# Kernel optimization log

Measured on AMD Instinct MI355X. Metric: run time of the kernel, lower is better.

## Reference

```python
import jax, jax.numpy as jnp
import numpy as np

D = 256      # input channels
DK = 64      # key/query/value channels
BS, W, H = 8, 64, 64


def setup_inputs() -> dict:
    key = jax.random.key(0)
    k1, k2, k3, k4 = jax.random.split(key, 4)
    v = jax.random.normal(k1, (BS, D, W, H), dtype=jnp.float32)
    # conv1x1 weights collapse to plain matrices over the channel dim
    Wqkv = jax.random.normal(k2, (3 * DK, D), dtype=jnp.float32) * 0.02
    Wout = jax.random.normal(k3, (D, DK), dtype=jnp.float32) * 0.02
    gamma = jax.random.normal(k4, (1,), dtype=jnp.float32)  # original inits to 0; nonzero for a non-degenerate baseline
    return {"v": v, "Wqkv": Wqkv, "Wout": Wout, "gamma": gamma}


def reference(v, Wqkv, Wout, gamma):
    bs, c, w, h = v.shape
    n = w * h
    d_k = Wout.shape[1]
    x = v.reshape(bs, c, n)                      # (b, c, n)
    qkv = jnp.einsum('oc,bcn->bon', Wqkv, x)      # 1x1 conv == channel matmul
    q = qkv[:, :d_k]                              # (b, dk, n)
    k = qkv[:, d_k:2 * d_k]
    val = qkv[:, 2 * d_k:]
    s = jnp.einsum('bdi,bdj->bij', q, k)          # (b, n, n) = query^T key
    beta = jax.nn.softmax(s, axis=2)              # exp(s - logsumexp(s, axis=2))
    y = jnp.einsum('bdi,bij->bdj', val, beta)     # bmm(value, beta)
    o = jnp.einsum('od,bdn->bon', Wout, y) * gamma[0] + x
    return o.reshape(bs, c, w, h)
```

## Files before the change

### kernel.cpp

```cpp
#include <hip/hip_runtime.h>

typedef unsigned short ushort_t;
typedef __bf16 bf16x8 __attribute__((ext_vector_type(8)));
typedef short short4v __attribute__((ext_vector_type(4)));
typedef float f32x4 __attribute__((ext_vector_type(4)));
typedef unsigned int uint4v __attribute__((ext_vector_type(4)));
typedef unsigned int uint2v __attribute__((ext_vector_type(2)));

#define NTOK 4096
#define DMODEL 256
#define DK 64
#define BS 8
#define LN2INV 1.44269504088896f

__device__ __forceinline__ ushort_t f2bf(float f) {
  unsigned u = __builtin_bit_cast(unsigned, f);
  u += 0x7fffu + ((u >> 16) & 1u);
  return (ushort_t)(u >> 16);
}
__device__ __forceinline__ float bf2f(ushort_t s) {
  return __builtin_bit_cast(float, ((unsigned)s) << 16);
}
__device__ __forceinline__ bf16x8 lds_frag(const ushort_t* p) {
  return __builtin_bit_cast(bf16x8, *(const uint4v*)p);
}
__device__ __forceinline__ float fexp2(float x) {
#if __has_builtin(__builtin_amdgcn_exp2f)
  return __builtin_amdgcn_exp2f(x);
#else
  return exp2f(x);
#endif
}
__device__ __forceinline__ unsigned bfpack(float x, float y) {
  return __builtin_amdgcn_perm(__builtin_bit_cast(unsigned, y),
                               __builtin_bit_cast(unsigned, x), 0x07060302u);
}
__device__ __forceinline__ f32x4 mfma16(short4v a, short4v b, f32x4 c) {
#if defined(__HIP_DEVICE_COMPILE__)
#if __has_builtin(__builtin_amdgcn_mfma_f32_16x16x16bf16_1k)
  return __builtin_amdgcn_mfma_f32_16x16x16bf16_1k(a, b, c, 0, 0, 0);
#else
  typedef __bf16 bf16x4 __attribute__((ext_vector_type(4)));
  return __builtin_amdgcn_mfma_f32_16x16x16_bf16(__builtin_bit_cast(bf16x4, a),
                                                 __builtin_bit_cast(bf16x4, b), c, 0, 0, 0);
#endif
#else
  (void)a; (void)b;
  return c;
#endif
}

__global__ __launch_bounds__(256) void k_convert(const float* __restrict__ Wqkv,
                                                 const float* __restrict__ Wout,
                                                 ushort_t* __restrict__ Wb,
                                                 ushort_t* __restrict__ Woutb) {
  int i = blockIdx.x * 256 + threadIdx.x;
  if (i < 3 * DK * DMODEL) {
    float w = Wqkv[i];
    if (i < DK * DMODEL) w *= LN2INV;
    Wb[i] = f2bf(w);
  } else {
    int j = i - 3 * DK * DMODEL;
    Woutb[j] = f2bf(Wout[j]);
  }
}

__global__ __launch_bounds__(256) void k_transpose(const float* __restrict__ x,
                                                   ushort_t* __restrict__ xT) {
  const int b = blockIdx.z;
  const int c0 = blockIdx.y * 64;
  const int n0 = blockIdx.x * 64;
  const int tid = threadIdx.x;
  __shared__ __align__(16) ushort_t t[64 * 72];
  const float* xb = x + (size_t)b * DMODEL * NTOK;
  ushort_t* xTb = xT + (size_t)b * NTOK * DMODEL;
#pragma unroll
  for (int kr = 0; kr < 2; kr++) {
    int s = tid + 256 * kr;
    int c = s >> 3, ns = (s & 7) * 8;
    const float* src = xb + (size_t)(c0 + c) * NTOK + n0 + ns;
    f32x4 a = *(const f32x4*)src;
    f32x4 bq = *(const f32x4*)(src + 4);
    uint4v o;
    o.x = (unsigned)f2bf(a[0]) | ((unsigned)f2bf(a[1]) << 16);
    o.y = (unsigned)f2bf(a[2]) | ((unsigned)f2bf(a[3]) << 16);
    o.z = (unsigned)f2bf(bq[0]) | ((unsigned)f2bf(bq[1]) << 16);
    o.w = (unsigned)f2bf(bq[2]) | ((unsigned)f2bf(bq[3]) << 16);
    *(uint4v*)(t + c * 72 + ns) = o;
  }
  __syncthreads();
#pragma unroll
  for (int kr = 0; kr < 2; kr++) {
    int s = tid + 256 * kr;
    int n = s >> 3, cs = (s & 7) * 8;
    unsigned e0 = t[(cs + 0) * 72 + n], e1 = t[(cs + 1) * 72 + n];
    unsigned e2 = t[(cs + 2) * 72 + n], e3 = t[(cs + 3) * 72 + n];
    unsigned e4 = t[(cs + 4) * 72 + n], e5 = t[(cs + 5) * 72 + n];
    unsigned e6 = t[(cs + 6) * 72 + n], e7 = t[(cs + 7) * 72 + n];
    uint4v o;
    o.x = e0 | (e1 << 16); o.y = e2 | (e3 << 16);
    o.z = e4 | (e5 << 16); o.w = e6 | (e7 << 16);
    *(uint4v*)(xTb + (size_t)(n0 + n) * DMODEL + c0 + cs) = o;
  }
}

__global__ __launch_bounds__(256) void k_qkv(const ushort_t* __restrict__ xT,
                                             const ushort_t* __restrict__ W,
                                             ushort_t* __restrict__ QT,
                                             ushort_t* __restrict__ KT,
                                             ushort_t* __restrict__ Vv) {
  const int b = blockIdx.y;
  const int n0 = blockIdx.x * 64;
  const int tid = threadIdx.x;
  const int lane = tid & 63, wv = tid >> 6;
  const int quad = lane >> 4, l15 = lane & 15;
  __shared__ __align__(16) ushort_t lw[192 * 40];
  __shared__ __align__(16) ushort_t lx[64 * 40];
  f32x4 acc[3][4];
  const f32x4 zero4 = {0.f, 0.f, 0.f, 0.f};
#pragma unroll
  for (int i = 0; i < 3; i++)
#pragma unroll
    for (int j = 0; j < 4; j++) acc[i][j] = zero4;

  const ushort_t* xTb = xT + ((size_t)b * NTOK + n0) * DMODEL;

  for (int c0 = 0; c0 < DMODEL; c0 += 32) {
    __syncthreads();
#pragma unroll
    for (int kr = 0; kr < 3; kr++) {
      int s = tid + 256 * kr;
      int o = s >> 2, cs = (s & 3) * 8;
      *(uint4v*)(lw + o * 40 + cs) = *(const uint4v*)(W + o * DMODEL + c0 + cs);
    }
    {
      int n = tid >> 2, cs = (tid & 3) * 8;
      *(uint4v*)(lx + n * 40 + cs) = *(const uint4v*)(xTb + (size_t)n * DMODEL + c0 + cs);
    }
    __syncthreads();
    bf16x8 bb[4];
#pragma unroll
    for (int nt = 0; nt < 4; nt++) bb[nt] = lds_frag(lx + (nt * 16 + l15) * 40 + quad * 8);
#pragma unroll
    for (int mt = 0; mt < 3; mt++) {
      bf16x8 a = lds_frag(lw + (wv * 48 + mt * 16 + l15) * 40 + quad * 8);
#pragma unroll
      for (int nt = 0; nt < 4; nt++)
        acc[mt][nt] = __builtin_amdgcn_mfma_f32_16x16x32_bf16(a, bb[nt], acc[mt][nt], 0, 0, 0);
    }
  }
#pragma unroll
  for (int mt = 0; mt < 3; mt++) {
    int o = wv * 48 + mt * 16 + quad * 4;
#pragma unroll
    for (int nt = 0; nt < 4; nt++) {
      int n = n0 + nt * 16 + l15;
      f32x4 v4 = acc[mt][nt];
      if (o < 128) {
        ushort_t* dst = (o < 64) ? (QT + ((size_t)b * NTOK + n) * DK + o)
                                 : (KT + ((size_t)b * NTOK + n) * DK + (o - 64));
        uint2v ww;
        ww.x = (unsigned)f2bf(v4[0]) | ((unsigned)f2bf(v4[1]) << 16);
        ww.y = (unsigned)f2bf(v4[2]) | ((unsigned)f2bf(v4[3]) << 16);
        *(uint2v*)dst = ww;
      } else {
        int d = o - 128;
#pragma unroll
        for (int r = 0; r < 4; r++)
          Vv[((size_t)b * DK + d + r) * NTOK + n] = f2bf(v4[r]);
      }
    }
  }
}

__global__ __launch_bounds__(256) void k_rsum(const ushort_t* __restrict__ QT,
                                              const ushort_t* __restrict__ KT,
                                              float* __restrict__ Rp) {
  const int id = blockIdx.x;
  const int b = id & 7;
  const int rest = id >> 3;
  const int i0 = (rest & 63) * 64;
  const int jh = rest >> 6;
  const int tid = threadIdx.x;
  const int lane = tid & 63, wv = tid >> 6;
  const int quad = lane >> 4, l15 = lane & 15;
  __shared__ __align__(16) ushort_t lq[64 * 72];
  __shared__ __align__(16) ushort_t lk[2][64 * 72];
  const ushort_t* QTb = QT + ((size_t)b * NTOK + i0) * DK;
  const ushort_t* KTb = KT + ((size_t)b * NTOK + jh * 2048) * DK;
#pragma unroll
  for (int kr = 0; kr < 2; kr++) {
    int s = tid + 256 * kr;
    int row = s >> 3, ds = (s & 7) * 8;
    *(uint4v*)(lq + row * 72 + ds) = *(const uint4v*)(QTb + (size_t)row * DK + ds);
    *(uint4v*)(lk[0] + row * 72 + ds) = *(const uint4v*)(KTb + (size_t)row * DK + ds);
  }
  __syncthreads();
  bf16x8 a0 = lds_frag(lq + (wv * 16 + l15) * 72 + quad * 8);
  bf16x8 a1 = lds_frag(lq + (wv * 16 + l15) * 72 + 32 + quad * 8);
  float lsum0 = 0.f, lsum1 = 0.f, lsum2 = 0.f, lsum3 = 0.f;
  const f32x4 zero4 = {0.f, 0.f, 0.f, 0.f};
  for (int it = 0; it < 32; it++) {
    if (it + 1 < 32) {
      const ushort_t* src = KTb + (size_t)(it + 1) * 64 * DK;
      ushort_t* dstb = lk[(it + 1) & 1];
#pragma unroll
      for (int kr = 0; kr < 2; kr++) {
        int s = tid + 256 * kr;
        int row = s >> 3, ds = (s & 7) * 8;
        *(uint4v*)(dstb + row * 72 + ds) = *(const uint4v*)(src + (size_t)row * DK + ds);
      }
    }
    const ushort_t* kb = lk[it & 1];
#pragma unroll
    for (int nt = 0; nt < 4; nt++) {
      bf16x8 b0 = lds_frag(kb + (nt * 16 + l15) * 72 + quad * 8);
      bf16x8 b1 = lds_frag(kb + (nt * 16 + l15) * 72 + 32 + quad * 8);
      f32x4 s4 = __builtin_amdgcn_mfma_f32_16x16x32_bf16(a0, b0, zero4, 0, 0, 0);
      s4 = __builtin_amdgcn_mfma_f32_16x16x32_bf16(a1, b1, s4, 0, 0, 0);
      lsum0 += fexp2(s4[0]);
      lsum1 += fexp2(s4[1]);
      lsum2 += fexp2(s4[2]);
      lsum3 += fexp2(s4[3]);
    }
    __syncthreads();
  }
#pragma unroll
  for (int off = 1; off < 16; off <<= 1) {
    lsum0 += __shfl_xor(lsum0, off);
    lsum1 += __shfl_xor(lsum1, off);
    lsum2 += __shfl_xor(lsum2, off);
    lsum3 += __shfl_xor(lsum3, off);
  }
  if (l15 < 4) {
    float v = (l15 == 0) ? lsum0 : (l15 == 1) ? lsum1 : (l15 == 2) ? lsum2 : lsum3;
    Rp[((size_t)(jh * 8 + b)) * NTOK + i0 + wv * 16 + quad * 4 + l15] = v;
  }
}

__global__ __launch_bounds__(256) void k_rmerge(const float* __restrict__ Rp,
                                                float* __restrict__ Rr) {
  int g = blockIdx.x * 256 + threadIdx.x;
  Rr[g] = 1.0f / (Rp[g] + Rp[BS * NTOK + g]);
}

__global__ __launch_bounds__(256) void k_pv(const ushort_t* __restrict__ QT,
                                            const ushort_t* __restrict__ KT,
                                            const ushort_t* __restrict__ Vv,
                                            const float* __restrict__ Rr,
                                            ushort_t* __restrict__ Yp) {
  const int id = blockIdx.x;
  const int b = id & 7;
  const int rest = id >> 3;
  const int j0 = (rest & 63) * 64;
  const int ih = rest >> 6;
  const int tid = threadIdx.x;
  const int lane = tid & 63, wv = tid >> 6;
  const int quad = lane >> 4, l15 = lane & 15;

  __shared__ __align__(16) ushort_t pool[18432];
#define LQ(buf) (pool + (buf) * 4608)
#define LV(buf) (pool + 9216 + (buf) * 4608)
  float* rbuf = (float*)pool;
  ushort_t* pbuf = pool + 8704;

  const ushort_t* KTb = KT + ((size_t)b * NTOK + j0) * DK;
  const ushort_t* QTb = QT + ((size_t)b * NTOK + ih * 2048) * DK;
  const ushort_t* Vbb = Vv + (size_t)b * DK * NTOK + ih * 2048;
  const float* Rrb = Rr + (size_t)b * NTOK + ih * 2048;

#pragma unroll
  for (int kr = 0; kr < 2; kr++) {
    int s = tid + 256 * kr;
    int row = s >> 3, ds = (s & 7) * 8;
    *(uint4v*)(LQ(0) + row * 72 + ds) = *(const uint4v*)(KTb + (size_t)row * DK + ds);
  }
  __syncthreads();
  bf16x8 kb0[4], kb1[4];
#pragma unroll
  for (int nt = 0; nt < 4; nt++) {
    kb0[nt] = lds_frag(LQ(0) + (nt * 16 + l15) * 72 + quad * 8);
    kb1[nt] = lds_frag(LQ(0) + (nt * 16 + l15) * 72 + 32 + quad * 8);
  }
  __syncthreads();
#pragma unroll
  for (int kr = 0; kr < 2; kr++) {
    int s = tid + 256 * kr;
    int row = s >> 3, ds = (s & 7) * 8;
    *(uint4v*)(LQ(0) + row * 72 + ds) = *(const uint4v*)(QTb + (size_t)row * DK + ds);
    *(uint4v*)(LV(0) + row * 72 + ds) = *(const uint4v*)(Vbb + (size_t)row * NTOK + ds);
  }
  __syncthreads();

  const f32x4 zero4 = {0.f, 0.f, 0.f, 0.f};
  f32x4 yt[4][4];
#pragma unroll
  for (int i = 0; i < 4; i++)
#pragma unroll
    for (int j = 0; j < 4; j++) yt[i][j] = zero4;

  for (int it = 0; it < 32; it++) {
    const int cb = it & 1, nb = cb ^ 1;
    f32x4 rv = *(const f32x4*)(Rrb + it * 64 + wv * 16 + quad * 4);
    if (it + 1 < 32) {
      const ushort_t* qsrc = QTb + (size_t)(it + 1) * 64 * DK;
#pragma unroll
      for (int kr = 0; kr < 2; kr++) {
        int s = tid + 256 * kr;
        int row = s >> 3, ds = (s & 7) * 8;
        *(uint4v*)(LQ(nb) + row * 72 + ds) = *(const uint4v*)(qsrc + (size_t)row * DK + ds);
        *(uint4v*)(LV(nb) + row * 72 + ds) =
            *(const uint4v*)(Vbb + (size_t)row * NTOK + (it + 1) * 64 + ds);
      }
    }
    bf16x8 a0 = lds_frag(LQ(cb) + (wv * 16 + l15) * 72 + quad * 8);
    bf16x8 a1 = lds_frag(LQ(cb) + (wv * 16 + l15) * 72 + 32 + quad * 8);
    short4v vf[4];
#pragma unroll
    for (int dsub = 0; dsub < 4; dsub++)
      vf[dsub] = __builtin_bit_cast(short4v,
          *(const uint2v*)(LV(cb) + (dsub * 16 + l15) * 72 + wv * 16 + quad * 4));
#pragma unroll
    for (int nt = 0; nt < 4; nt++) {
      f32x4 s4 = __builtin_amdgcn_mfma_f32_16x16x32_bf16(a0, kb0[nt], zero4, 0, 0, 0);
      s4 = __builtin_amdgcn_mfma_f32_16x16x32_bf16(a1, kb1[nt], s4, 0, 0, 0);
      uint2v wp;
      wp.x = bfpack(fexp2(s4[0]) * rv[0], fexp2(s4[1]) * rv[1]);
      wp.y = bfpack(fexp2(s4[2]) * rv[2], fexp2(s4[3]) * rv[3]);
      short4v wf = __builtin_bit_cast(short4v, wp);
#pragma unroll
      for (int dsub = 0; dsub < 4; dsub++)
        yt[nt][dsub] = mfma16(wf, vf[dsub], yt[nt][dsub]);
    }
    __syncthreads();
  }

  if (wv == 0) {
#pragma unroll
    for (int nt = 0; nt < 4; nt++)
#pragma unroll
      for (int dsub = 0; dsub < 4; dsub++)
        *(f32x4*)(rbuf + (dsub * 16 + l15) * 68 + nt * 16 + quad * 4) = yt[nt][dsub];
  }
  __syncthreads();
  if (wv == 1) {
#pragma unroll
    for (int nt = 0; nt < 4; nt++)
#pragma unroll
      for (int dsub = 0; dsub < 4; dsub++) {
        float* p = rbuf + (dsub * 16 + l15) * 68 + nt * 16 + quad * 4;
        *(f32x4*)p = *(const f32x4*)p + yt[nt][dsub];
      }
  }
  __syncthreads();
  if (wv == 2) {
#pragma unroll
    for (int nt = 0; nt < 4; nt++)
#pragma unroll
      for (int dsub = 0; dsub < 4; dsub++) {
        float* p = rbuf + (dsub * 16 + l15) * 68 + nt * 16 + quad * 4;
        *(f32x4*)p = *(const f32x4*)p + yt[nt][dsub];
      }
  }
  __syncthreads();
  if (wv == 3) {
#pragma unroll
    for (int nt = 0; nt < 4; nt++)
#pragma unroll
      for (int dsub = 0; dsub < 4; dsub++) {
        const float* p = rbuf + (dsub * 16 + l15) * 68 + nt * 16 + quad * 4;
        f32x4 v4 = *(const f32x4*)p + yt[nt][dsub];
#pragma unroll
        for (int r = 0; r < 4; r++)
          pbuf[(nt * 16 + quad * 4 + r) * 72 + dsub * 16 + l15] = f2bf(v4[r]);
      }
  }
  __syncthreads();

  ushort_t* Ypb = Yp + ((size_t)(ih * 8 + b) * NTOK + j0) * DK;
#pragma unroll
  for (int kr = 0; kr < 2; kr++) {
    int s = tid + 256 * kr;
    int row = s >> 3, c8 = (s & 7) * 8;
    *(uint4v*)(Ypb + (size_t)row * DK + c8) = *(const uint4v*)(pbuf + row * 72 + c8);
  }
#undef LQ
#undef LV
}

__global__ __launch_bounds__(256) void k_out(const ushort_t* __restrict__ Yp,
                                             const ushort_t* __restrict__ Wout,
                                             const float* __restrict__ gammap,
                                             const float* __restrict__ x,
                                             float* __restrict__ outp) {
  const int id = blockIdx.x;
  const int b = id & 7;
  const int n0 = (id >> 3) * 64;
  const int tid = threadIdx.x;
  const int lane = tid & 63, wv = tid >> 6;
  const int quad = lane >> 4, l15 = lane & 15;
  __shared__ __align__(16) ushort_t pbuf[64 * 72];

  const ushort_t* Y0 = Yp + ((size_t)b * NTOK + n0) * DK;
  const ushort_t* Y1 = Yp + ((size_t)(8 + b) * NTOK + n0) * DK;
#pragma unroll
  for (int kr = 0; kr < 2; kr++) {
    int s = tid + 256 * kr;
    int row = s >> 3, c8 = (s & 7) * 8;
    uint4v ua = *(const uint4v*)(Y0 + (size_t)row * DK + c8);
    uint4v ub = *(const uint4v*)(Y1 + (size_t)row * DK + c8);
    uint4v oc;
    unsigned* pa = (unsigned*)&ua;
    unsigned* pb = (unsigned*)&ub;
    unsigned* po = (unsigned*)&oc;
#pragma unroll
    for (int w = 0; w < 4; w++) {
      float lo = bf2f((ushort_t)(pa[w] & 0xffff)) + bf2f((ushort_t)(pb[w] & 0xffff));
      float hi = bf2f((ushort_t)(pa[w] >> 16)) + bf2f((ushort_t)(pb[w] >> 16));
      po[w] = bfpack(lo, hi);
    }
    *(uint4v*)(pbuf + row * 72 + c8) = oc;
  }
  __syncthreads();

  const f32x4 zero4 = {0.f, 0.f, 0.f, 0.f};
  bf16x8 yb0[4], yb1[4];
#pragma unroll
  for (int nt = 0; nt < 4; nt++) {
    yb0[nt] = lds_frag(pbuf + (nt * 16 + l15) * 72 + quad * 8);
    yb1[nt] = lds_frag(pbuf + (nt * 16 + l15) * 72 + 32 + quad * 8);
  }
  f32x4 oacc[4][4];
#pragma unroll
  for (int m = 0; m < 4; m++)
#pragma unroll
    for (int nt = 0; nt < 4; nt++) oacc[m][nt] = zero4;
#pragma unroll
  for (int m = 0; m < 4; m++) {
    int c = (wv * 4 + m) * 16 + l15;
    bf16x8 aw0 = __builtin_bit_cast(bf16x8, *(const uint4v*)(Wout + c * DK + quad * 8));
    bf16x8 aw1 = __builtin_bit_cast(bf16x8, *(const uint4v*)(Wout + c * DK + 32 + quad * 8));
#pragma unroll
    for (int nt = 0; nt < 4; nt++) {
      oacc[m][nt] = __builtin_amdgcn_mfma_f32_16x16x32_bf16(aw0, yb0[nt], oacc[m][nt], 0, 0, 0);
      oacc[m][nt] = __builtin_amdgcn_mfma_f32_16x16x32_bf16(aw1, yb1[nt], oacc[m][nt], 0, 0, 0);
    }
  }
  float g = gammap[0];
  const float* xb = x + (size_t)b * DMODEL * NTOK;
  float* ob = outp + (size_t)b * DMODEL * NTOK;
#pragma unroll
  for (int m = 0; m < 4; m++) {
    int cbase = (wv * 4 + m) * 16 + quad * 4;
#pragma unroll
    for (int nt = 0; nt < 4; nt++) {
      int n = n0 + nt * 16 + l15;
#pragma unroll
      for (int r = 0; r < 4; r++) {
        size_t idx = (size_t)(cbase + r) * NTOK + n;
        ob[idx] = oacc[m][nt][r] * g + xb[idx];
      }
    }
  }
}

extern "C" void kernel_launch(void* const* d_in, const int* in_sizes, int n_in,
                              void* d_out, int out_size, void* d_ws, size_t ws_size,
                              hipStream_t stream) {
  const float* v = (const float*)d_in[0];
  const float* Wqkv = (const float*)d_in[1];
  const float* Wout = (const float*)d_in[2];
  const float* gamma = (const float*)d_in[3];
  float* outp = (float*)d_out;

  ushort_t* xT = (ushort_t*)d_ws;
  ushort_t* QT = xT + (size_t)BS * NTOK * DMODEL;
  ushort_t* KT = QT + (size_t)BS * NTOK * DK;
  ushort_t* Vs = KT + (size_t)BS * NTOK * DK;
  ushort_t* Wb = Vs + (size_t)BS * DK * NTOK;
  ushort_t* Woutb = Wb + 3 * DK * DMODEL;
  float* Rp = (float*)(Woutb + DMODEL * DK);
  float* Rr = Rp + 2 * (size_t)BS * NTOK;
  ushort_t* Yp = (ushort_t*)(Rr + (size_t)BS * NTOK);

  k_convert<<<dim3(256), 256, 0, stream>>>(Wqkv, Wout, Wb, Woutb);
  k_transpose<<<dim3(64, 4, BS), 256, 0, stream>>>(v, xT);
  k_qkv<<<dim3(64, BS), 256, 0, stream>>>(xT, Wb, QT, KT, Vs);
  k_rsum<<<dim3(1024), 256, 0, stream>>>(QT, KT, Rp);
  k_rmerge<<<dim3(128), 256, 0, stream>>>(Rp, Rr);
  k_pv<<<dim3(1024), 256, 0, stream>>>(QT, KT, Vs, Rr, Yp);
  k_out<<<dim3(512), 256, 0, stream>>>(Yp, Woutb, gamma, v, outp);
}
```

Before: 215.8 us.

## Fold softmax row normalisation into V, enlarge rsum tiles, interleave batch blocks

Row-sum reciprocals are merged and multiplied into V in a new k_rv kernel, so k_pv no longer loads R and scales each exp by it. This removes a global load and multiplies from the hot attention loop. k_rsum now handles 128 query rows per block, reusing each K tile over twice as many rows. The double-buffer loops in k_rsum and k_pv are unrolled by two with fixed buffer indices, and transpose/qkv grids are flattened with the batch index in the low bits. Scaling V per key token in bf16 adds an extra rounding step and an in-place pass over V.

After: 228.1 us. 1.06x slower.

```diff
diff --git a/kernel.cpp b/kernel.cpp
--- a/kernel.cpp
+++ b/kernel.cpp
@@ -67,9 +67,11 @@
 
 __global__ __launch_bounds__(256) void k_transpose(const float* __restrict__ x,
                                                    ushort_t* __restrict__ xT) {
-  const int b = blockIdx.z;
-  const int c0 = blockIdx.y * 64;
-  const int n0 = blockIdx.x * 64;
+  const int id = blockIdx.x;
+  const int b = id & 7;
+  const int rest = id >> 3;
+  const int c0 = (rest & 3) * 64;
+  const int n0 = (rest >> 2) * 64;
   const int tid = threadIdx.x;
   __shared__ __align__(16) ushort_t t[64 * 72];
   const float* xb = x + (size_t)b * DMODEL * NTOK;
@@ -109,8 +111,9 @@
                                              ushort_t* __restrict__ QT,
                                              ushort_t* __restrict__ KT,
                                              ushort_t* __restrict__ Vv) {
-  const int b = blockIdx.y;
-  const int n0 = blockIdx.x * 64;
+  const int id = blockIdx.x;
+  const int b = id & 7;
+  const int n0 = (id >> 3) * 64;
   const int tid = threadIdx.x;
   const int lane = tid & 63, wv = tid >> 6;
   const int quad = lane >> 4, l15 = lane & 15;
@@ -179,75 +182,125 @@
   const int id = blockIdx.x;
   const int b = id & 7;
   const int rest = id >> 3;
-  const int i0 = (rest & 63) * 64;
-  const int jh = rest >> 6;
+  const int i0 = (rest & 31) * 128;
+  const int jh = rest >> 5;
   const int tid = threadIdx.x;
   const int lane = tid & 63, wv = tid >> 6;
   const int quad = lane >> 4, l15 = lane & 15;
-  __shared__ __align__(16) ushort_t lq[64 * 72];
+  __shared__ __align__(16) ushort_t lq[128 * 72];
   __shared__ __align__(16) ushort_t lk[2][64 * 72];
   const ushort_t* QTb = QT + ((size_t)b * NTOK + i0) * DK;
   const ushort_t* KTb = KT + ((size_t)b * NTOK + jh * 2048) * DK;
 #pragma unroll
-  for (int kr = 0; kr < 2; kr++) {
+  for (int kr = 0; kr < 4; kr++) {
     int s = tid + 256 * kr;
     int row = s >> 3, ds = (s & 7) * 8;
     *(uint4v*)(lq + row * 72 + ds) = *(const uint4v*)(QTb + (size_t)row * DK + ds);
+  }
+#pragma unroll
+  for (int kr = 0; kr < 2; kr++) {
+    int s = tid + 256 * kr;
+    int row = s >> 3, ds = (s & 7) * 8;
     *(uint4v*)(lk[0] + row * 72 + ds) = *(const uint4v*)(KTb + (size_t)row * DK + ds);
   }
   __syncthreads();
-  bf16x8 a0 = lds_frag(lq + (wv * 16 + l15) * 72 + quad * 8);
-  bf16x8 a1 = lds_frag(lq + (wv * 16 + l15) * 72 + 32 + quad * 8);
-  float lsum0 = 0.f, lsum1 = 0.f, lsum2 = 0.f, lsum3 = 0.f;
+  bf16x8 aa[2][2];
+#pragma unroll
+  for (int isub = 0; isub < 2; isub++) {
+    aa[isub][0] = lds_frag(lq + (wv * 32 + isub * 16 + l15) * 72 + quad * 8);
+    aa[isub][1] = lds_frag(lq + (wv * 32 + isub * 16 + l15) * 72 + 32 + quad * 8);
+  }
+  float lsum[2][4];
+#pragma unroll
+  for (int i = 0; i < 2; i++)
+#pragma unroll
+    for (int r = 0; r < 4; r++) lsum[i][r] = 0.f;
   const f32x4 zero4 = {0.f, 0.f, 0.f, 0.f};
-  for (int it = 0; it < 32; it++) {
-    if (it + 1 < 32) {
-      const ushort_t* src = KTb + (size_t)(it + 1) * 64 * DK;
-      ushort_t* dstb = lk[(it + 1) & 1];
-#pragma unroll
-      for (int kr = 0; kr < 2; kr++) {
-        int s = tid + 256 * kr;
-        int row = s >> 3, ds = (s & 7) * 8;
-        *(uint4v*)(dstb + row * 72 + ds) = *(const uint4v*)(src + (size_t)row * DK + ds);
-      }
-    }
-    const ushort_t* kb = lk[it & 1];
+
+  auto stage = [&](ushort_t* dstb, int itn) {
+    const ushort_t* src = KTb + (size_t)itn * 64 * DK;
+#pragma unroll
+    for (int kr = 0; kr < 2; kr++) {
+      int s = tid + 256 * kr;
+      int row = s >> 3, ds = (s & 7) * 8;
+      *(uint4v*)(dstb + row * 72 + ds) = *(const uint4v*)(src + (size_t)row * DK + ds);
+    }
+  };
+  auto body = [&](const ushort_t* kb) {
 #pragma unroll
     for (int nt = 0; nt < 4; nt++) {
       bf16x8 b0 = lds_frag(kb + (nt * 16 + l15) * 72 + quad * 8);
       bf16x8 b1 = lds_frag(kb + (nt * 16 + l15) * 72 + 32 + quad * 8);
-      f32x4 s4 = __builtin_amdgcn_mfma_f32_16x16x32_bf16(a0, b0, zero4, 0, 0, 0);
-      s4 = __builtin_amdgcn_mfma_f32_16x16x32_bf16(a1, b1, s4, 0, 0, 0);
-      lsum0 += fexp2(s4[0]);
-      lsum1 += fexp2(s4[1]);
-      lsum2 += fexp2(s4[2]);
-      lsum3 += fexp2(s4[3]);
-    }
+#pragma unroll
+      for (int isub = 0; isub < 2; isub++) {
+        f32x4 s4 = __builtin_amdgcn_mfma_f32_16x16x32_bf16(aa[isub][0], b0, zero4, 0, 0, 0);
+        s4 = __builtin_amdgcn_mfma_f32_16x16x32_bf16(aa[isub][1], b1, s4, 0, 0, 0);
+        lsum[isub][0] += fexp2(s4[0]);
+        lsum[isub][1] += fexp2(s4[1]);
+        lsum[isub][2] += fexp2(s4[2]);
+        lsum[isub][3] += fexp2(s4[3]);
+      }
+    }
+  };
+
+  for (int it2 = 0; it2 < 16; it2++) {
+    int it = it2 * 2;
+    stage(lk[1], it + 1);
+    body(lk[0]);
     __syncthreads();
-  }
-#pragma unroll
-  for (int off = 1; off < 16; off <<= 1) {
-    lsum0 += __shfl_xor(lsum0, off);
-    lsum1 += __shfl_xor(lsum1, off);
-    lsum2 += __shfl_xor(lsum2, off);
-    lsum3 += __shfl_xor(lsum3, off);
-  }
-  if (l15 < 4) {
-    float v = (l15 == 0) ? lsum0 : (l15 == 1) ? lsum1 : (l15 == 2) ? lsum2 : lsum3;
-    Rp[((size_t)(jh * 8 + b)) * NTOK + i0 + wv * 16 + quad * 4 + l15] = v;
-  }
-}
-
-__global__ __launch_bounds__(256) void k_rmerge(const float* __restrict__ Rp,
-                                                float* __restrict__ Rr) {
-  int g = blockIdx.x * 256 + threadIdx.x;
-  Rr[g] = 1.0f / (Rp[g] + Rp[BS * NTOK + g]);
+    if (it2 < 15) stage(lk[0], it + 2);
+    body(lk[1]);
+    __syncthreads();
+  }
+
+#pragma unroll
+  for (int isub = 0; isub < 2; isub++)
+#pragma unroll
+    for (int r = 0; r < 4; r++)
+#pragma unroll
+      for (int off = 1; off < 16; off <<= 1) lsum[isub][r] += __shfl_xor(lsum[isub][r], off);
+  if (l15 < 8) {
+    int rr = l15 & 3, isub = l15 >> 2;
+    float va = (rr == 0) ? lsum[0][0] : (rr == 1) ? lsum[0][1] : (rr == 2) ? lsum[0][2] : lsum[0][3];
+    float vb = (rr == 0) ? lsum[1][0] : (rr == 1) ? lsum[1][1] : (rr == 2) ? lsum[1][2] : lsum[1][3];
+    float v = isub ? vb : va;
+    Rp[((size_t)(jh * 8 + b)) * NTOK + i0 + wv * 32 + isub * 16 + quad * 4 + rr] = v;
+  }
+}
+
+__global__ __launch_bounds__(256) void k_rv(const float* __restrict__ Rp,
+                                            ushort_t* __restrict__ Vv) {
+  const int id = blockIdx.x;
+  const int b = id & 7;
+  const int ibase = (id >> 3) * 256;
+  const int tid = threadIdx.x;
+  __shared__ float lrr[256];
+  size_t g = (size_t)b * NTOK + ibase + tid;
+  lrr[tid] = 1.0f / (Rp[g] + Rp[(size_t)8 * NTOK + g]);
+  __syncthreads();
+  const int dsub = tid >> 5;
+  const int ioff = (tid & 31) * 8;
+#pragma unroll
+  for (int d8 = 0; d8 < 8; d8++) {
+    int d = d8 * 8 + dsub;
+    ushort_t* vp = Vv + ((size_t)b * DK + d) * NTOK + ibase + ioff;
+    uint4v v0 = *(const uint4v*)vp;
+    uint4v o0;
+    unsigned* vi = (unsigned*)&v0;
+    unsigned* oo = (unsigned*)&o0;
+#pragma unroll
+    for (int w = 0; w < 4; w++) {
+      float e0 = bf2f((ushort_t)(vi[w] & 0xffff)) * lrr[ioff + 2 * w];
+      float e1 = bf2f((ushort_t)(vi[w] >> 16)) * lrr[ioff + 2 * w + 1];
+      oo[w] = (unsigned)f2bf(e0) | ((unsigned)f2bf(e1) << 16);
+    }
+    *(uint4v*)vp = o0;
+  }
 }
 
 __global__ __launch_bounds__(256) void k_pv(const ushort_t* __restrict__ QT,
                                             const ushort_t* __restrict__ KT,
                                             const ushort_t* __restrict__ Vv,
-                                            const float* __restrict__ Rr,
                                             ushort_t* __restrict__ Yp) {
   const int id = blockIdx.x;
   const int b = id & 7;
@@ -267,7 +320,6 @@
   const ushort_t* KTb = KT + ((size_t)b * NTOK + j0) * DK;
   const ushort_t* QTb = QT + ((size_t)b * NTOK + ih * 2048) * DK;
   const ushort_t* Vbb = Vv + (size_t)b * DK * NTOK + ih * 2048;
-  const float* Rrb = Rr + (size_t)b * NTOK + ih * 2048;
 
 #pragma unroll
   for (int kr = 0; kr < 2; kr++) {
@@ -299,39 +351,46 @@
 #pragma unroll
     for (int j = 0; j < 4; j++) yt[i][j] = zero4;
 
-  for (int it = 0; it < 32; it++) {
-    const int cb = it & 1, nb = cb ^ 1;
-    f32x4 rv = *(const f32x4*)(Rrb + it * 64 + wv * 16 + quad * 4);
-    if (it + 1 < 32) {
-      const ushort_t* qsrc = QTb + (size_t)(it + 1) * 64 * DK;
-#pragma unroll
-      for (int kr = 0; kr < 2; kr++) {
-        int s = tid + 256 * kr;
-        int row = s >> 3, ds = (s & 7) * 8;
-        *(uint4v*)(LQ(nb) + row * 72 + ds) = *(const uint4v*)(qsrc + (size_t)row * DK + ds);
-        *(uint4v*)(LV(nb) + row * 72 + ds) =
-            *(const uint4v*)(Vbb + (size_t)row * NTOK + (it + 1) * 64 + ds);
-      }
-    }
-    bf16x8 a0 = lds_frag(LQ(cb) + (wv * 16 + l15) * 72 + quad * 8);
-    bf16x8 a1 = lds_frag(LQ(cb) + (wv * 16 + l15) * 72 + 32 + quad * 8);
+  auto stage = [&](ushort_t* lqn, ushort_t* lvn, int itn) {
+    const ushort_t* qsrc = QTb + (size_t)itn * 64 * DK;
+    const ushort_t* vsrc = Vbb + itn * 64;
+#pragma unroll
+    for (int kr = 0; kr < 2; kr++) {
+      int s = tid + 256 * kr;
+      int row = s >> 3, ds = (s & 7) * 8;
+      *(uint4v*)(lqn + row * 72 + ds) = *(const uint4v*)(qsrc + (size_t)row * DK + ds);
+      *(uint4v*)(lvn + row * 72 + ds) = *(const uint4v*)(vsrc + (size_t)row * NTOK + ds);
+    }
+  };
+  auto body = [&](const ushort_t* lqc, const ushort_t* lvc) {
+    bf16x8 a0 = lds_frag(lqc + (wv * 16 + l15) * 72 + quad * 8);
+    bf16x8 a1 = lds_frag(lqc + (wv * 16 + l15) * 72 + 32 + quad * 8);
     short4v vf[4];
 #pragma unroll
     for (int dsub = 0; dsub < 4; dsub++)
       vf[dsub] = __builtin_bit_cast(short4v,
-          *(const uint2v*)(LV(cb) + (dsub * 16 + l15) * 72 + wv * 16 + quad * 4));
+          *(const uint2v*)(lvc + (dsub * 16 + l15) * 72 + wv * 16 + quad * 4));
 #pragma unroll
     for (int nt = 0; nt < 4; nt++) {
       f32x4 s4 = __builtin_amdgcn_mfma_f32_16x16x32_bf16(a0, kb0[nt], zero4, 0, 0, 0);
       s4 = __builtin_amdgcn_mfma_f32_16x16x32_bf16(a1, kb1[nt], s4, 0, 0, 0);
       uint2v wp;
-      wp.x = bfpack(fexp2(s4[0]) * rv[0], fexp2(s4[1]) * rv[1]);
-      wp.y = bfpack(fexp2(s4[2]) * rv[2], fexp2(s4[3]) * rv[3]);
+      wp.x = bfpack(fexp2(s4[0]), fexp2(s4[1]));
+      wp.y = bfpack(fexp2(s4[2]), fexp2(s4[3]));
       short4v wf = __builtin_bit_cast(short4v, wp);
 #pragma unroll
       for (int dsub = 0; dsub < 4; dsub++)
         yt[nt][dsub] = mfma16(wf, vf[dsub], yt[nt][dsub]);
     }
+  };
+
+  for (int it2 = 0; it2 < 16; it2++) {
+    int it = it2 * 2;
+    stage(LQ(1), LV(1), it + 1);
+    body(LQ(0), LV(0));
+    __syncthreads();
+    if (it2 < 15) stage(LQ(0), LV(0), it + 2);
+    body(LQ(1), LV(1));
     __syncthreads();
   }
 
@@ -480,14 +539,13 @@
   ushort_t* Wb = Vs + (size_t)BS * DK * NTOK;
   ushort_t* Woutb = Wb + 3 * DK * DMODEL;
   float* Rp = (float*)(Woutb + DMODEL * DK);
-  float* Rr = Rp + 2 * (size_t)BS * NTOK;
-  ushort_t* Yp = (ushort_t*)(Rr + (size_t)BS * NTOK);
+  ushort_t* Yp = (ushort_t*)(Rp + 2 * (size_t)BS * NTOK);
 
   k_convert<<<dim3(256), 256, 0, stream>>>(Wqkv, Wout, Wb, Woutb);
-  k_transpose<<<dim3(64, 4, BS), 256, 0, stream>>>(v, xT);
-  k_qkv<<<dim3(64, BS), 256, 0, stream>>>(xT, Wb, QT, KT, Vs);
-  k_rsum<<<dim3(1024), 256, 0, stream>>>(QT, KT, Rp);
-  k_rmerge<<<dim3(128), 256, 0, stream>>>(Rp, Rr);
-  k_pv<<<dim3(1024), 256, 0, stream>>>(QT, KT, Vs, Rr, Yp);
+  k_transpose<<<dim3(2048), 256, 0, stream>>>(v, xT);
+  k_qkv<<<dim3(512), 256, 0, stream>>>(xT, Wb, QT, KT, Vs);
+  k_rsum<<<dim3(512), 256, 0, stream>>>(QT, KT, Rp);
+  k_rv<<<dim3(128), 256, 0, stream>>>(Rp, Vs);
+  k_pv<<<dim3(1024), 256, 0, stream>>>(QT, KT, Vs, Yp);
   k_out<<<dim3(512), 256, 0, stream>>>(Yp, Woutb, gamma, v, outp);
 }
```
